# Performance work log

Hardware: AMD Instinct MI355X
Metric: run time of the kernel (lower is better)

Reference implementation:

```python
import jax, jax.numpy as jnp
import numpy as np

TEMPERATURE = 0.02


def setup_inputs() -> dict:
    key = jax.random.key(0)
    k1, k2 = jax.random.split(key)
    B, D_PER, DIM = 4096, 2, 1024
    # scale embeddings so sim/temperature stays in a sane range (like normalized embeddings)
    scale = 1.0 / np.sqrt(DIM)
    query_embeds = jax.random.normal(k1, (B, DIM), dtype=jnp.float32) * scale
    doc_embeds = jax.random.normal(k2, (B * D_PER, DIM), dtype=jnp.float32) * scale
    return {
        "query_embeds": query_embeds,
        "doc_embeds": doc_embeds,
        "num_docs_per_sample": D_PER,
    }


def reference(query_embeds, doc_embeds, num_docs_per_sample):
    # Single-device path of the original: all_doc_embeds == doc_embeds,
    # local_rank == 0, pos_global_idx = i * num_docs_per_sample.
    B = query_embeds.shape[0]
    # [B, total_docs] similarity matrix (one batched GEMM instead of per-sample loop)
    logits = (query_embeds @ doc_embeds.T) / TEMPERATURE
    pos_idx = jnp.arange(B) * num_docs_per_sample  # constant docs-per-sample offsets
    pos_logit = jnp.take_along_axis(logits, pos_idx[:, None], axis=1)[:, 0]
    lse = jax.nn.logsumexp(logits, axis=1)
    loss = jnp.sum(lse - pos_logit) / B
    return loss
```

## Files before the change

kernel.cpp:

```cpp
#include <hip/hip_runtime.h>


#define TEMP_INV 50.0f
#define PRESCALE 16.0f
#define SCALE_BYTE 123

typedef int   i32x4 __attribute__((ext_vector_type(4)));
typedef int   i32x8 __attribute__((ext_vector_type(8)));
typedef float f32x4 __attribute__((ext_vector_type(4)));

__global__ void cvt_kernel(const float* __restrict__ Q, const float* __restrict__ Dm,
                           unsigned int* __restrict__ Q8, unsigned int* __restrict__ D8,
                           float* __restrict__ rowsum, int qSlots, int B, int K) {
    const int gid = blockIdx.x * blockDim.x + threadIdx.x;
    if (gid < B) rowsum[gid] = 0.0f;
    const float* src;
    unsigned int* dst;
    int s;
    if (gid < qSlots) { src = Q;  dst = Q8; s = gid; }
    else              { src = Dm; dst = D8; s = gid - qSlots; }
    const int l   = s & 63;
    const int c   = (s >> 6) & 15;
    const int k0b = (s >> 10) & 7;
    const int R   = s >> 13;
    const int row = R * 128 + (c >> 1) * 16 + (l & 15);
    const int k   = k0b * 128 + (c & 1) * 64 + (l >> 4) * 16;
    const float* p = src + (size_t)row * K + k;
    unsigned int w[4];
#pragma unroll
    for (int d = 0; d < 4; ++d) {
        float4 v = *(const float4*)(p + d * 4);
        int t = __builtin_amdgcn_cvt_pk_fp8_f32(v.x * PRESCALE, v.y * PRESCALE, 0, false);
        t = __builtin_amdgcn_cvt_pk_fp8_f32(v.z * PRESCALE, v.w * PRESCALE, t, true);
        w[d] = (unsigned int)t;
    }
    *(uint4*)(dst + (size_t)s * 4) = make_uint4(w[0], w[1], w[2], w[3]);
}

__global__ __launch_bounds__(256, 2) void gemm_expsum_kernel(
        const unsigned int* __restrict__ Q8, const unsigned int* __restrict__ D8,
        const int* __restrict__ dper,
        float* __restrict__ rowsum, float* __restrict__ pos, int K) {
    __shared__ unsigned int Qs[4096];
    __shared__ unsigned int Ds[4096];

    const int tid   = threadIdx.x;
    const int wave  = tid >> 6;
    const int lane  = tid & 63;
    const int lquad = lane >> 4;
    const int lm    = lane & 15;
    const int qbase = blockIdx.x * 128;
    const int dbase = blockIdx.y * 128;
    const int KB    = K >> 7;

    const int slotofs = ((lquad & 1) * 32 + lm) * 4;
    const int aofs = ((wave >> 1) * 8 + (lquad >> 1)) * 256 + slotofs;
    const int bofs = ((wave & 1) * 8 + (lquad >> 1)) * 256 + slotofs;

    const unsigned int* Qg = Q8 + (size_t)blockIdx.x * KB * 4096;
    const unsigned int* Dg = D8 + (size_t)blockIdx.y * KB * 4096;

    f32x4 acc[16];
#pragma unroll
    for (int t = 0; t < 16; ++t) acc[t] = (f32x4){0.f, 0.f, 0.f, 0.f};

    for (int kb = 0; kb < KB; ++kb) {
#pragma unroll
        for (int q = 0; q < 4; ++q) {
            const int c = wave * 4 + q;
            const unsigned int* g1 = Qg + kb * 4096 + c * 256 + lane * 4;
            __builtin_amdgcn_global_load_lds(
                (const __attribute__((address_space(1))) void*)g1,
                (__attribute__((address_space(3))) void*)(Qs + c * 256 + lane * 4),
                16, 0, 0);
            const unsigned int* g2 = Dg + kb * 4096 + c * 256 + lane * 4;
            __builtin_amdgcn_global_load_lds(
                (const __attribute__((address_space(1))) void*)g2,
                (__attribute__((address_space(3))) void*)(Ds + c * 256 + lane * 4),
                16, 0, 0);
        }
        __syncthreads();

        i32x8 a8[4], b8[4];
#pragma unroll
        for (int i = 0; i < 4; ++i) {
            i32x4 lo = *(const i32x4*)(Qs + aofs + i * 512);
            i32x4 hi = *(const i32x4*)(Qs + aofs + i * 512 + 64);
            a8[i] = __builtin_shufflevector(lo, hi, 0, 1, 2, 3, 4, 5, 6, 7);
        }
#pragma unroll
        for (int j = 0; j < 4; ++j) {
            i32x4 lo = *(const i32x4*)(Ds + bofs + j * 512);
            i32x4 hi = *(const i32x4*)(Ds + bofs + j * 512 + 64);
            b8[j] = __builtin_shufflevector(lo, hi, 0, 1, 2, 3, 4, 5, 6, 7);
        }
#pragma unroll
        for (int i = 0; i < 4; ++i)
#pragma unroll
            for (int j = 0; j < 4; ++j)
                acc[i * 4 + j] = __builtin_amdgcn_mfma_scale_f32_16x16x128_f8f6f4(
                    a8[i], b8[j], acc[i * 4 + j], 0, 0, 0, SCALE_BYTE, 0, SCALE_BYTE);
        __syncthreads();
    }

    const int dp = dper[0];
#pragma unroll
    for (int i = 0; i < 4; ++i)
#pragma unroll
        for (int r = 0; r < 4; ++r) {
            const int gr   = qbase + (wave >> 1) * 64 + 16 * i + 4 * lquad + r;
            const int pcol = gr * dp - dbase;
            float e = 0.0f;
#pragma unroll
            for (int j = 0; j < 4; ++j) {
                float v = acc[i * 4 + j][r];
                if ((wave & 1) * 64 + 16 * j + lm == pcol) pos[gr] = v * TEMP_INV;
                e += __expf(v * TEMP_INV);
            }
            e += __shfl_xor(e, 1);
            e += __shfl_xor(e, 2);
            e += __shfl_xor(e, 4);
            e += __shfl_xor(e, 8);
            if (lm == 0) atomicAdd(&rowsum[gr], e);
        }
}

__global__ void final_kernel(const float* __restrict__ rowsum,
                             const float* __restrict__ pos,
                             float* __restrict__ out, int B) {
    __shared__ float red[16];
    int tid = threadIdx.x;
    float s = 0.0f;
    for (int i = tid; i < B; i += blockDim.x)
        s += __logf(rowsum[i]) - pos[i];
    s += __shfl_xor(s, 32);
    s += __shfl_xor(s, 16);
    s += __shfl_xor(s, 8);
    s += __shfl_xor(s, 4);
    s += __shfl_xor(s, 2);
    s += __shfl_xor(s, 1);
    int w = tid >> 6, l = tid & 63;
    if (l == 0) red[w] = s;
    __syncthreads();
    if (tid == 0) {
        float t = 0.0f;
        int nw = blockDim.x >> 6;
        for (int i = 0; i < nw; ++i) t += red[i];
        out[0] = t / (float)B;
    }
}

extern "C" void kernel_launch(void* const* d_in, const int* in_sizes, int n_in,
                              void* d_out, int out_size, void* d_ws, size_t ws_size,
                              hipStream_t stream) {
    const float* Q   = (const float*)d_in[0];
    const float* Dm  = (const float*)d_in[1];
    const int* dper  = (const int*)d_in[2];
    float* out = (float*)d_out;

    const int DIM  = 1024;
    const int B    = in_sizes[0] / DIM;
    const int Ntot = in_sizes[1] / DIM;

    unsigned int* Q8 = (unsigned int*)d_ws;
    unsigned int* D8 = Q8 + (size_t)B * DIM / 4;
    float* rowsum = (float*)(D8 + (size_t)Ntot * DIM / 4);
    float* pos = rowsum + B;

    const int qSlots = B * DIM / 16;
    const int dSlots = Ntot * DIM / 16;
    cvt_kernel<<<(qSlots + dSlots) / 256, 256, 0, stream>>>(
        Q, Dm, Q8, D8, rowsum, qSlots, B, DIM);

    dim3 grid(B / 128, Ntot / 128);
    gemm_expsum_kernel<<<grid, 256, 0, stream>>>(Q8, D8, dper, rowsum, pos, DIM);

    final_kernel<<<1, 1024, 0, stream>>>(rowsum, pos, out, B);
}
```

Measured before the change: 127.7 us.

## Fuse final reduction into GEMM via last-block counter and coalesce cvt reads

Removes the separate final_kernel launch by having each GEMM block bump a global counter after its atomics. The last block to finish reads rowsum and pos and computes the loss. The conversion kernel now maps threads to contiguous input floats, so global reads are coalesced, and it scatters writes into the tiled FP8 layout instead of the reverse. This trades one kernel launch and uncoalesced reads for a per-block fence and atomic, plus a serial tail reduction in one block.

```diff
diff --git a/kernel.cpp b/kernel.cpp
--- a/kernel.cpp
+++ b/kernel.cpp
@@ -4,6 +4,7 @@
 #define TEMP_INV 50.0f
 #define PRESCALE 16.0f
 #define SCALE_BYTE 123
+#define KD 1024
 
 typedef int   i32x4 __attribute__((ext_vector_type(4)));
 typedef int   i32x8 __attribute__((ext_vector_type(8)));
@@ -11,21 +12,27 @@
 
 __global__ void cvt_kernel(const float* __restrict__ Q, const float* __restrict__ Dm,
                            unsigned int* __restrict__ Q8, unsigned int* __restrict__ D8,
-                           float* __restrict__ rowsum, int qSlots, int B, int K) {
+                           float* __restrict__ rowsum, unsigned int* __restrict__ cnt,
+                           int qThreads, int B) {
     const int gid = blockIdx.x * blockDim.x + threadIdx.x;
     if (gid < B) rowsum[gid] = 0.0f;
+    if (gid == 0) cnt[0] = 0u;
     const float* src;
     unsigned int* dst;
-    int s;
-    if (gid < qSlots) { src = Q;  dst = Q8; s = gid; }
-    else              { src = Dm; dst = D8; s = gid - qSlots; }
-    const int l   = s & 63;
-    const int c   = (s >> 6) & 15;
-    const int k0b = (s >> 10) & 7;
-    const int R   = s >> 13;
-    const int row = R * 128 + (c >> 1) * 16 + (l & 15);
-    const int k   = k0b * 128 + (c & 1) * 64 + (l >> 4) * 16;
-    const float* p = src + (size_t)row * K + k;
+    int f;
+    if (gid < qThreads) { src = Q;  dst = Q8; f = gid * 16; }
+    else                { src = Dm; dst = D8; f = (gid - qThreads) * 16; }
+    const int r  = f >> 10;
+    const int kk = f & 1023;
+    const int k0b = kk >> 7;
+    const int kh  = (kk >> 6) & 1;
+    const int kq  = (kk >> 4) & 3;
+    const int R   = r >> 7;
+    const int rg  = (r >> 4) & 7;
+    const int lr  = r & 15;
+    const size_t off = (size_t)(R * 8 + k0b) * 4096 + (rg * 2 + kh) * 256
+                     + (kq * 16 + lr) * 4;
+    const float* p = src + (size_t)f;
     unsigned int w[4];
 #pragma unroll
     for (int d = 0; d < 4; ++d) {
@@ -34,15 +41,19 @@
         t = __builtin_amdgcn_cvt_pk_fp8_f32(v.z * PRESCALE, v.w * PRESCALE, t, true);
         w[d] = (unsigned int)t;
     }
-    *(uint4*)(dst + (size_t)s * 4) = make_uint4(w[0], w[1], w[2], w[3]);
+    *(uint4*)(dst + off) = make_uint4(w[0], w[1], w[2], w[3]);
 }
 
 __global__ __launch_bounds__(256, 2) void gemm_expsum_kernel(
         const unsigned int* __restrict__ Q8, const unsigned int* __restrict__ D8,
         const int* __restrict__ dper,
-        float* __restrict__ rowsum, float* __restrict__ pos, int K) {
+        float* __restrict__ rowsum, float* __restrict__ pos,
+        unsigned int* __restrict__ cnt, float* __restrict__ out,
+        int B, int K) {
     __shared__ unsigned int Qs[4096];
     __shared__ unsigned int Ds[4096];
+    __shared__ float redf[4];
+    __shared__ int amLastS;
 
     const int tid   = threadIdx.x;
     const int wave  = tid >> 6;
@@ -123,30 +134,34 @@
             e += __shfl_xor(e, 8);
             if (lm == 0) atomicAdd(&rowsum[gr], e);
         }
-}
 
-__global__ void final_kernel(const float* __restrict__ rowsum,
-                             const float* __restrict__ pos,
-                             float* __restrict__ out, int B) {
-    __shared__ float red[16];
-    int tid = threadIdx.x;
-    float s = 0.0f;
-    for (int i = tid; i < B; i += blockDim.x)
-        s += __logf(rowsum[i]) - pos[i];
-    s += __shfl_xor(s, 32);
-    s += __shfl_xor(s, 16);
-    s += __shfl_xor(s, 8);
-    s += __shfl_xor(s, 4);
-    s += __shfl_xor(s, 2);
-    s += __shfl_xor(s, 1);
-    int w = tid >> 6, l = tid & 63;
-    if (l == 0) red[w] = s;
     __syncthreads();
     if (tid == 0) {
-        float t = 0.0f;
-        int nw = blockDim.x >> 6;
-        for (int i = 0; i < nw; ++i) t += red[i];
-        out[0] = t / (float)B;
+        __threadfence();
+        unsigned int old = __hip_atomic_fetch_add(cnt, 1u, __ATOMIC_ACQ_REL,
+                                                  __HIP_MEMORY_SCOPE_AGENT);
+        amLastS = (old == gridDim.x * gridDim.y - 1) ? 1 : 0;
+    }
+    __syncthreads();
+    if (amLastS) {
+        float s = 0.0f;
+        for (int i = tid; i < B; i += 256) {
+            float rs = __hip_atomic_load(&rowsum[i], __ATOMIC_RELAXED,
+                                         __HIP_MEMORY_SCOPE_AGENT);
+            float ps = __hip_atomic_load(&pos[i], __ATOMIC_RELAXED,
+                                         __HIP_MEMORY_SCOPE_AGENT);
+            s += __logf(rs) - ps;
+        }
+        s += __shfl_xor(s, 32);
+        s += __shfl_xor(s, 16);
+        s += __shfl_xor(s, 8);
+        s += __shfl_xor(s, 4);
+        s += __shfl_xor(s, 2);
+        s += __shfl_xor(s, 1);
+        if (lane == 0) redf[wave] = s;
+        __syncthreads();
+        if (tid == 0)
+            out[0] = (redf[0] + redf[1] + redf[2] + redf[3]) / (float)B;
     }
 }
 
@@ -158,7 +173,7 @@
     const int* dper  = (const int*)d_in[2];
     float* out = (float*)d_out;
 
-    const int DIM  = 1024;
+    const int DIM  = KD;
     const int B    = in_sizes[0] / DIM;
     const int Ntot = in_sizes[1] / DIM;
 
@@ -166,14 +181,14 @@
     unsigned int* D8 = Q8 + (size_t)B * DIM / 4;
     float* rowsum = (float*)(D8 + (size_t)Ntot * DIM / 4);
     float* pos = rowsum + B;
+    unsigned int* cnt = (unsigned int*)(pos + B);
 
-    const int qSlots = B * DIM / 16;
-    const int dSlots = Ntot * DIM / 16;
-    cvt_kernel<<<(qSlots + dSlots) / 256, 256, 0, stream>>>(
-        Q, Dm, Q8, D8, rowsum, qSlots, B, DIM);
+    const int qThreads = B * DIM / 16;
+    const int dThreads = Ntot * DIM / 16;
+    cvt_kernel<<<(qThreads + dThreads) / 256, 256, 0, stream>>>(
+        Q, Dm, Q8, D8, rowsum, cnt, qThreads, B);
 
     dim3 grid(B / 128, Ntot / 128);
-    gemm_expsum_kernel<<<grid, 256, 0, stream>>>(Q8, D8, dper, rowsum, pos, DIM);
-
-    final_kernel<<<1, 1024, 0, stream>>>(rowsum, pos, out, B);
+    gemm_expsum_kernel<<<grid, 256, 0, stream>>>(Q8, D8, dper, rowsum, pos,
+                                                 cnt, out, B, DIM);
 }
```

New measurement: 199.3 us. +56.1%, slower.

## Enlarge GEMM block tile to 128x256 with eight waves per block

Applied to the files above, without the earlier changes.

The block tile of the FP8 GEMM grows from 128x128 to 128x256. Blocks now run 512 threads (8 waves in a 2x4 arrangement), and the LDS buffer for the doc operand is doubled. Each loaded Q tile is reused across twice as many doc columns, which cuts global/L2 traffic per output and halves the grid size. The cost is more LDS per block, which may lower occupancy, and a grid of only 32x32 blocks, which may leave the machine less evenly loaded.

```diff
diff --git a/kernel.cpp b/kernel.cpp
--- a/kernel.cpp
+++ b/kernel.cpp
@@ -4,6 +4,7 @@
 #define TEMP_INV 50.0f
 #define PRESCALE 16.0f
 #define SCALE_BYTE 123
+#define KD 1024
 
 typedef int   i32x4 __attribute__((ext_vector_type(4)));
 typedef int   i32x8 __attribute__((ext_vector_type(8)));
@@ -37,28 +38,30 @@
     *(uint4*)(dst + (size_t)s * 4) = make_uint4(w[0], w[1], w[2], w[3]);
 }
 
-__global__ __launch_bounds__(256, 2) void gemm_expsum_kernel(
+__global__ __launch_bounds__(512, 2) void gemm_expsum_kernel(
         const unsigned int* __restrict__ Q8, const unsigned int* __restrict__ D8,
         const int* __restrict__ dper,
         float* __restrict__ rowsum, float* __restrict__ pos, int K) {
     __shared__ unsigned int Qs[4096];
-    __shared__ unsigned int Ds[4096];
+    __shared__ unsigned int Ds[8192];
 
     const int tid   = threadIdx.x;
     const int wave  = tid >> 6;
     const int lane  = tid & 63;
     const int lquad = lane >> 4;
     const int lm    = lane & 15;
+    const int wr    = wave >> 2;
+    const int wc    = wave & 3;
     const int qbase = blockIdx.x * 128;
-    const int dbase = blockIdx.y * 128;
+    const int dbase = blockIdx.y * 256;
     const int KB    = K >> 7;
 
     const int slotofs = ((lquad & 1) * 32 + lm) * 4;
-    const int aofs = ((wave >> 1) * 8 + (lquad >> 1)) * 256 + slotofs;
-    const int bofs = ((wave & 1) * 8 + (lquad >> 1)) * 256 + slotofs;
+    const int aofs = wr * 2048 + (lquad >> 1) * 256 + slotofs;
+    const int bofs = wc * 2048 + (lquad >> 1) * 256 + slotofs;
 
     const unsigned int* Qg = Q8 + (size_t)blockIdx.x * KB * 4096;
-    const unsigned int* Dg = D8 + (size_t)blockIdx.y * KB * 4096;
+    const unsigned int* Dg = D8 + (size_t)blockIdx.y * 2 * KB * 4096;
 
     f32x4 acc[16];
 #pragma unroll
@@ -66,18 +69,25 @@
 
     for (int kb = 0; kb < KB; ++kb) {
 #pragma unroll
-        for (int q = 0; q < 4; ++q) {
-            const int c = wave * 4 + q;
-            const unsigned int* g1 = Qg + kb * 4096 + c * 256 + lane * 4;
+        for (int q = 0; q < 6; ++q) {
+            const int c6 = wave * 6 + q;
+            const unsigned int* src;
+            unsigned int* dst;
+            if (c6 < 16) {
+                src = Qg + kb * 4096 + c6 * 256 + lane * 4;
+                dst = (unsigned int*)Qs + c6 * 256 + lane * 4;
+            } else if (c6 < 32) {
+                const int cc = c6 - 16;
+                src = Dg + kb * 4096 + cc * 256 + lane * 4;
+                dst = (unsigned int*)Ds + cc * 256 + lane * 4;
+            } else {
+                const int cc = c6 - 32;
+                src = Dg + (size_t)KB * 4096 + kb * 4096 + cc * 256 + lane * 4;
+                dst = (unsigned int*)Ds + 4096 + cc * 256 + lane * 4;
+            }
             __builtin_amdgcn_global_load_lds(
-                (const __attribute__((address_space(1))) void*)g1,
-                (__attribute__((address_space(3))) void*)(Qs + c * 256 + lane * 4),
-                16, 0, 0);
-            const unsigned int* g2 = Dg + kb * 4096 + c * 256 + lane * 4;
-            __builtin_amdgcn_global_load_lds(
-                (const __attribute__((address_space(1))) void*)g2,
-                (__attribute__((address_space(3))) void*)(Ds + c * 256 + lane * 4),
-                16, 0, 0);
+                (const __attribute__((address_space(1))) void*)src,
+                (__attribute__((address_space(3))) void*)dst, 16, 0, 0);
         }
         __syncthreads();
 
@@ -108,13 +118,13 @@
     for (int i = 0; i < 4; ++i)
 #pragma unroll
         for (int r = 0; r < 4; ++r) {
-            const int gr   = qbase + (wave >> 1) * 64 + 16 * i + 4 * lquad + r;
+            const int gr   = qbase + wr * 64 + 16 * i + 4 * lquad + r;
             const int pcol = gr * dp - dbase;
             float e = 0.0f;
 #pragma unroll
             for (int j = 0; j < 4; ++j) {
                 float v = acc[i * 4 + j][r];
-                if ((wave & 1) * 64 + 16 * j + lm == pcol) pos[gr] = v * TEMP_INV;
+                if (wc * 64 + 16 * j + lm == pcol) pos[gr] = v * TEMP_INV;
                 e += __expf(v * TEMP_INV);
             }
             e += __shfl_xor(e, 1);
@@ -158,7 +168,7 @@
     const int* dper  = (const int*)d_in[2];
     float* out = (float*)d_out;
 
-    const int DIM  = 1024;
+    const int DIM  = KD;
     const int B    = in_sizes[0] / DIM;
     const int Ntot = in_sizes[1] / DIM;
 
@@ -172,8 +182,8 @@
     cvt_kernel<<<(qSlots + dSlots) / 256, 256, 0, stream>>>(
         Q, Dm, Q8, D8, rowsum, qSlots, B, DIM);
 
-    dim3 grid(B / 128, Ntot / 128);
-    gemm_expsum_kernel<<<grid, 256, 0, stream>>>(Q8, D8, dper, rowsum, pos, DIM);
+    dim3 grid(B / 128, Ntot / 256);
+    gemm_expsum_kernel<<<grid, 512, 0, stream>>>(Q8, D8, dper, rowsum, pos, DIM);
 
     final_kernel<<<1, 1024, 0, stream>>>(rowsum, pos, out, B);
 }
```

New measurement: 149.8 us. +17.3%, slower.

## Double-buffer LDS tiles in FP8 GEMM to overlap global loads with MFMA

Applied to the files above, without the earlier changes.

Splits the Q and D shared-memory tiles into two buffers and issues the direct-to-LDS loads for the next K block before computing on the current one. The first block is prefetched before the loop, and one of the two barriers per iteration is removed. The goal is to hide global-load latency behind MFMA work. In exchange the kernel uses twice the LDS, and the overlap depends on the compiler not inserting a conservative memory wait before the LDS reads.

```diff
diff --git a/kernel.cpp b/kernel.cpp
--- a/kernel.cpp
+++ b/kernel.cpp
@@ -4,6 +4,7 @@
 #define TEMP_INV 50.0f
 #define PRESCALE 16.0f
 #define SCALE_BYTE 123
+#define KD 1024
 
 typedef int   i32x4 __attribute__((ext_vector_type(4)));
 typedef int   i32x8 __attribute__((ext_vector_type(8)));
@@ -41,8 +42,8 @@
         const unsigned int* __restrict__ Q8, const unsigned int* __restrict__ D8,
         const int* __restrict__ dper,
         float* __restrict__ rowsum, float* __restrict__ pos, int K) {
-    __shared__ unsigned int Qs[4096];
-    __shared__ unsigned int Ds[4096];
+    __shared__ unsigned int Qs[2][4096];
+    __shared__ unsigned int Ds[2][4096];
 
     const int tid   = threadIdx.x;
     const int wave  = tid >> 6;
@@ -60,38 +61,56 @@
     const unsigned int* Qg = Q8 + (size_t)blockIdx.x * KB * 4096;
     const unsigned int* Dg = D8 + (size_t)blockIdx.y * KB * 4096;
 
+    const int stg = (wave * 4) * 256 + lane * 4;
+
     f32x4 acc[16];
 #pragma unroll
     for (int t = 0; t < 16; ++t) acc[t] = (f32x4){0.f, 0.f, 0.f, 0.f};
 
+#pragma unroll
+    for (int q = 0; q < 4; ++q) {
+        __builtin_amdgcn_global_load_lds(
+            (const __attribute__((address_space(1))) void*)(Qg + stg + q * 256),
+            (__attribute__((address_space(3))) void*)(&Qs[0][0] + stg + q * 256),
+            16, 0, 0);
+        __builtin_amdgcn_global_load_lds(
+            (const __attribute__((address_space(1))) void*)(Dg + stg + q * 256),
+            (__attribute__((address_space(3))) void*)(&Ds[0][0] + stg + q * 256),
+            16, 0, 0);
+    }
+
     for (int kb = 0; kb < KB; ++kb) {
+        const int cur = kb & 1;
+        __syncthreads();
+
+        if (kb + 1 < KB) {
+            const int nxt = 1 - cur;
+            const unsigned int* Qn = Qg + (kb + 1) * 4096;
+            const unsigned int* Dn = Dg + (kb + 1) * 4096;
 #pragma unroll
-        for (int q = 0; q < 4; ++q) {
-            const int c = wave * 4 + q;
-            const unsigned int* g1 = Qg + kb * 4096 + c * 256 + lane * 4;
-            __builtin_amdgcn_global_load_lds(
-                (const __attribute__((address_space(1))) void*)g1,
-                (__attribute__((address_space(3))) void*)(Qs + c * 256 + lane * 4),
-                16, 0, 0);
-            const unsigned int* g2 = Dg + kb * 4096 + c * 256 + lane * 4;
-            __builtin_amdgcn_global_load_lds(
-                (const __attribute__((address_space(1))) void*)g2,
-                (__attribute__((address_space(3))) void*)(Ds + c * 256 + lane * 4),
-                16, 0, 0);
+            for (int q = 0; q < 4; ++q) {
+                __builtin_amdgcn_global_load_lds(
+                    (const __attribute__((address_space(1))) void*)(Qn + stg + q * 256),
+                    (__attribute__((address_space(3))) void*)(&Qs[nxt][0] + stg + q * 256),
+                    16, 0, 0);
+                __builtin_amdgcn_global_load_lds(
+                    (const __attribute__((address_space(1))) void*)(Dn + stg + q * 256),
+                    (__attribute__((address_space(3))) void*)(&Ds[nxt][0] + stg + q * 256),
+                    16, 0, 0);
+            }
         }
-        __syncthreads();
 
         i32x8 a8[4], b8[4];
 #pragma unroll
         for (int i = 0; i < 4; ++i) {
-            i32x4 lo = *(const i32x4*)(Qs + aofs + i * 512);
-            i32x4 hi = *(const i32x4*)(Qs + aofs + i * 512 + 64);
+            i32x4 lo = *(const i32x4*)(&Qs[cur][0] + aofs + i * 512);
+            i32x4 hi = *(const i32x4*)(&Qs[cur][0] + aofs + i * 512 + 64);
             a8[i] = __builtin_shufflevector(lo, hi, 0, 1, 2, 3, 4, 5, 6, 7);
         }
 #pragma unroll
         for (int j = 0; j < 4; ++j) {
-            i32x4 lo = *(const i32x4*)(Ds + bofs + j * 512);
-            i32x4 hi = *(const i32x4*)(Ds + bofs + j * 512 + 64);
+            i32x4 lo = *(const i32x4*)(&Ds[cur][0] + bofs + j * 512);
+            i32x4 hi = *(const i32x4*)(&Ds[cur][0] + bofs + j * 512 + 64);
             b8[j] = __builtin_shufflevector(lo, hi, 0, 1, 2, 3, 4, 5, 6, 7);
         }
 #pragma unroll
@@ -100,7 +119,6 @@
             for (int j = 0; j < 4; ++j)
                 acc[i * 4 + j] = __builtin_amdgcn_mfma_scale_f32_16x16x128_f8f6f4(
                     a8[i], b8[j], acc[i * 4 + j], 0, 0, 0, SCALE_BYTE, 0, SCALE_BYTE);
-        __syncthreads();
     }
 
     const int dp = dper[0];
@@ -158,7 +176,7 @@
     const int* dper  = (const int*)d_in[2];
     float* out = (float*)d_out;
 
-    const int DIM  = 1024;
+    const int DIM  = KD;
     const int B    = in_sizes[0] / DIM;
     const int Ntot = in_sizes[1] / DIM;
 
```

New measurement: 137.7 us. +7.9%, slower.
